# Performance work log

Hardware: AMD Instinct MI355X
Metric: run time of the kernel (lower is better)

## Reference

```python
import jax, jax.numpy as jnp
import numpy as np

NEG_SLOPE = 0.01  # torch.nn.LeakyReLU default


def setup_inputs() -> dict:
    key = jax.random.key(0)
    k1, k2, k3, k4, k5 = jax.random.split(key, 5)
    n_nodes, n_sources, d_in, d_out = 20000, 2048, 128, 128
    x = jax.random.normal(k1, (n_nodes, d_in), dtype=jnp.float32)
    A = jax.random.normal(k2, (n_nodes, n_sources), dtype=jnp.float32)
    W = jax.random.normal(k3, (d_in, d_in), dtype=jnp.float32) * (1.0 / np.sqrt(d_in))
    dense0_w = jax.random.normal(k4, (d_out, d_in), dtype=jnp.float32) * (1.0 / np.sqrt(d_in))
    src_idx = jnp.sort(jax.random.randint(k5, (n_sources,), 0, n_nodes, dtype=jnp.int64))
    return {"x": x, "A": A, "W": W, "dense0_w": dense0_w, "src_idx": src_idx}


def reference(x, A, W, dense0_w, src_idx):
    # GCNConv_Fixed_W: gather source nodes, shared weight transform, adjacency matmul
    support = x[src_idx] @ W                 # [n_sources, d_in]
    out = A @ support                        # [n_nodes, d_in]
    # nonlin + stacked Linear (1 layer, no bias)
    out = jnp.where(out >= 0, out, NEG_SLOPE * out)  # LeakyReLU
    out = out @ dense0_w.T                   # [n_nodes, d_out]
    return out
```

## Files before the change

### kernel.cpp

```cpp
#include <hip/hip_runtime.h>
#include <stdint.h>

#define NNODES 20000
#define NSRC   2048
#define DIN    128
#define BM     80

typedef short s16x8 __attribute__((ext_vector_type(8)));
typedef unsigned short u16x8 __attribute__((ext_vector_type(8)));
typedef float f32x4 __attribute__((ext_vector_type(4)));

static __device__ __forceinline__ unsigned short f2bf(float f) {
  union { float f; unsigned int u; } v; v.f = f;
  unsigned int r = v.u + 0x7FFFu + ((v.u >> 16) & 1u);
  return (unsigned short)(r >> 16);
}

static __device__ __forceinline__ s16x8 pack8(float4 a, float4 b) {
  s16x8 r;
  r[0] = (short)f2bf(a.x); r[1] = (short)f2bf(a.y);
  r[2] = (short)f2bf(a.z); r[3] = (short)f2bf(a.w);
  r[4] = (short)f2bf(b.x); r[5] = (short)f2bf(b.y);
  r[6] = (short)f2bf(b.z); r[7] = (short)f2bf(b.w);
  return r;
}

static __device__ __forceinline__ s16x8 load_cvt8(const float* __restrict__ p) {
  return pack8(*reinterpret_cast<const float4*>(p),
               *reinterpret_cast<const float4*>(p + 4));
}

#define GLL16(g, l)                                                          \
  __builtin_amdgcn_global_load_lds(                                          \
      (const __attribute__((address_space(1))) void*)(g),                    \
      (__attribute__((address_space(3))) void*)(l), 16, 0, 0)

__global__ __launch_bounds__(128) void support_kernel(
    const float* __restrict__ x, const float* __restrict__ W,
    const int* __restrict__ src_idx, unsigned short* __restrict__ supTp) {
  __shared__ float xrows[8][DIN];
  const int j = threadIdx.x;
  const int s0 = blockIdx.x * 8;
#pragma unroll
  for (int i = 0; i < 8; ++i) {
    const int src = src_idx[s0 + i];
    xrows[i][j] = x[(size_t)src * DIN + j];
  }
  __syncthreads();
  float acc[8];
#pragma unroll
  for (int i = 0; i < 8; ++i) acc[i] = 0.f;
  for (int k = 0; k < DIN; ++k) {
    const float w = W[(size_t)k * DIN + j];
#pragma unroll
    for (int i = 0; i < 8; ++i) acc[i] += xrows[i][k] * w;
  }
  u16x8 o;
#pragma unroll
  for (int i = 0; i < 8; ++i) o[i] = f2bf(acc[i]);
  const int kk = s0 >> 5;
  const int g2 = (s0 >> 3) & 3;
  const int n = j >> 4;
  const int lane = (j & 15) + g2 * 16;
  *reinterpret_cast<u16x8*>(&supTp[(size_t)((kk * 8 + n) * 64 + lane) * 8]) = o;
}

__global__ __launch_bounds__(320) void fused_gcn_kernel(
    const float* __restrict__ A,
    const unsigned short* __restrict__ supTp,
    const float* __restrict__ Wd,
    float* __restrict__ out) {
  const int tid = threadIdx.x;
  const int lane = tid & 63;
  const int w = tid >> 6;
  const int r16 = lane & 15;
  const int g = lane >> 4;
  const int rowBase = blockIdx.x * BM;

  __shared__ __attribute__((aligned(16))) unsigned char pool[73728];
  float* Ap = (float*)pool;
  unsigned short* Bp = (unsigned short*)(pool + 40960);

  f32x4 acc[8];
#pragma unroll
  for (int n = 0; n < 8; ++n) acc[n] = (f32x4){0.f, 0.f, 0.f, 0.f};

  const int wu = __builtin_amdgcn_readfirstlane(w);

#define STAGE(buf, c)                                                         \
  {                                                                           \
    _Pragma("unroll") for (int i2 = 0; i2 < 4; ++i2) {                        \
      const int i = w * 4 + i2;                                               \
      const int row = 4 * i + (lane >> 4);                                    \
      GLL16(A + (size_t)(rowBase + row) * NSRC + (c) * 64 +                   \
                (((lane & 15) ^ (row & 7)) << 2),                             \
            Ap + (buf) * 5120 + i * 256);                                     \
    }                                                                         \
    if (wu < 4) {                                                             \
      _Pragma("unroll") for (int i2 = 0; i2 < 4; ++i2) {                      \
        const int iB = w * 4 + i2;                                            \
        GLL16(supTp +                                                         \
                  ((size_t)(((c) * 2 + (iB >> 3)) * 8 + (iB & 7)) * 64 +      \
                   lane) * 8,                                                 \
              Bp + (buf) * 8192 + iB * 512);                                  \
      }                                                                       \
    }                                                                         \
  }

#define COMPUTE(buf)                                                          \
  {                                                                           \
    _Pragma("unroll") for (int kk2 = 0; kk2 < 2; ++kk2) {                     \
      const float* rb = Ap + (buf) * 5120 + (w * 16 + r16) * 64;              \
      const float4 lo = *reinterpret_cast<const float4*>(                     \
          &rb[((kk2 * 8 + g * 2) ^ (r16 & 7)) << 2]);                         \
      const float4 hi = *reinterpret_cast<const float4*>(                     \
          &rb[((kk2 * 8 + g * 2 + 1) ^ (r16 & 7)) << 2]);                     \
      const s16x8 a = pack8(lo, hi);                                          \
      _Pragma("unroll") for (int n = 0; n < 8; ++n) {                         \
        const s16x8 b = *reinterpret_cast<const s16x8*>(                      \
            &Bp[(buf) * 8192 + ((kk2 * 8 + n) * 64 + lane) * 8]);             \
        acc[n] =                                                              \
            __builtin_amdgcn_mfma_f32_16x16x32_bf16(a, b, acc[n], 0, 0, 0);   \
      }                                                                       \
    }                                                                         \
  }

  STAGE(0, 0);
  for (int c = 0; c < 31; ++c) {
    STAGE((c & 1) ^ 1, c + 1);
    if (wu < 4) {
      asm volatile("s_waitcnt vmcnt(8)" ::: "memory");
    } else {
      asm volatile("s_waitcnt vmcnt(4)" ::: "memory");
    }
    __builtin_amdgcn_s_barrier();
    COMPUTE(c & 1);
    __builtin_amdgcn_s_barrier();
  }
  asm volatile("s_waitcnt vmcnt(0)" ::: "memory");
  __builtin_amdgcn_s_barrier();
  COMPUTE(1);

  __builtin_amdgcn_s_barrier();
  unsigned short* actw = (unsigned short*)pool + w * 2176;
#pragma unroll
  for (int n = 0; n < 8; ++n)
#pragma unroll
    for (int r = 0; r < 4; ++r) {
      float v = acc[n][r];
      v = (v >= 0.f) ? v : 0.01f * v;
      actw[(g * 4 + r) * 136 + n * 16 + r16] = f2bf(v);
    }

  f32x4 acc2[8];
#pragma unroll
  for (int n = 0; n < 8; ++n) acc2[n] = (f32x4){0.f, 0.f, 0.f, 0.f};
#pragma unroll
  for (int k2 = 0; k2 < 4; ++k2) {
    const int k = k2 * 32 + g * 8;
    const s16x8 a2 = *reinterpret_cast<const s16x8*>(&actw[r16 * 136 + k]);
#pragma unroll
    for (int n = 0; n < 8; ++n) {
      const s16x8 b2 = load_cvt8(Wd + (size_t)(n * 16 + r16) * DIN + k);
      acc2[n] =
          __builtin_amdgcn_mfma_f32_16x16x32_bf16(a2, b2, acc2[n], 0, 0, 0);
    }
  }
#pragma unroll
  for (int n = 0; n < 8; ++n)
#pragma unroll
    for (int r = 0; r < 4; ++r)
      out[(size_t)(rowBase + w * 16 + g * 4 + r) * DIN + n * 16 + r16] =
          acc2[n][r];
}

extern "C" void kernel_launch(void* const* d_in, const int* in_sizes, int n_in,
                              void* d_out, int out_size, void* d_ws, size_t ws_size,
                              hipStream_t stream) {
  const float* x   = (const float*)d_in[0];
  const float* A   = (const float*)d_in[1];
  const float* W   = (const float*)d_in[2];
  const float* Wd  = (const float*)d_in[3];
  const int*   src = (const int*)d_in[4];
  float* out = (float*)d_out;

  unsigned short* supTp = (unsigned short*)d_ws;

  support_kernel<<<NSRC / 8, 128, 0, stream>>>(x, W, src, supTp);
  fused_gcn_kernel<<<NNODES / BM, 320, 0, stream>>>(A, supTp, Wd, out);
}
```

Measured before the change: 66.55 us.

## Split the A@support K dimension across two blocks and combine in a second kernel

The fused kernel is split into a split-K kernel and a combine kernel. Each of 500 blocks handles half of the 2048-wide K dimension for an 80-row tile, starting at a staggered chunk offset to spread memory traffic. Partial sums are written to workspace as bf16, and a new combine kernel adds the two halves, applies LeakyReLU and runs the dense projection. This doubles the block count from 250 to 500, which helps fill the GPU's compute units. The cost is an extra kernel launch, a workspace round trip, and rounding the partial sums to bf16 before they are added.

```diff
diff --git a/kernel.cpp b/kernel.cpp
--- a/kernel.cpp
+++ b/kernel.cpp
@@ -4,7 +4,8 @@
 #define NNODES 20000
 #define NSRC   2048
 #define DIN    128
-#define BM     80
+#define NTILE  250
+#define TW     5
 
 typedef short s16x8 __attribute__((ext_vector_type(8)));
 typedef unsigned short u16x8 __attribute__((ext_vector_type(8)));
@@ -14,6 +15,11 @@
   union { float f; unsigned int u; } v; v.f = f;
   unsigned int r = v.u + 0x7FFFu + ((v.u >> 16) & 1u);
   return (unsigned short)(r >> 16);
+}
+
+static __device__ __forceinline__ float bf2f(unsigned short u) {
+  union { unsigned int u; float f; } v; v.u = ((unsigned int)u) << 16;
+  return v.f;
 }
 
 static __device__ __forceinline__ s16x8 pack8(float4 a, float4 b) {
@@ -65,17 +71,20 @@
   *reinterpret_cast<u16x8*>(&supTp[(size_t)((kk * 8 + n) * 64 + lane) * 8]) = o;
 }
 
-__global__ __launch_bounds__(320) void fused_gcn_kernel(
+__global__ __launch_bounds__(320) void splitk_kernel(
     const float* __restrict__ A,
     const unsigned short* __restrict__ supTp,
-    const float* __restrict__ Wd,
-    float* __restrict__ out) {
+    unsigned short* __restrict__ pws) {
   const int tid = threadIdx.x;
   const int lane = tid & 63;
   const int w = tid >> 6;
   const int r16 = lane & 15;
   const int g = lane >> 4;
-  const int rowBase = blockIdx.x * BM;
+  const int bid = blockIdx.x;
+  const int tile = bid >> 1;
+  const int half = bid & 1;
+  const int rowBase = tile * 80;
+  const int off = bid & 15;
 
   __shared__ __attribute__((aligned(16))) unsigned char pool[73728];
   float* Ap = (float*)pool;
@@ -87,21 +96,21 @@
 
   const int wu = __builtin_amdgcn_readfirstlane(w);
 
-#define STAGE(buf, c)                                                         \
+#define STAGE(buf, cc)                                                        \
   {                                                                           \
     _Pragma("unroll") for (int i2 = 0; i2 < 4; ++i2) {                        \
-      const int i = w * 4 + i2;                                               \
-      const int row = 4 * i + (lane >> 4);                                    \
-      GLL16(A + (size_t)(rowBase + row) * NSRC + (c) * 64 +                   \
+      const int row = w * 16 + i2 * 4 + (lane >> 4);                          \
+      GLL16(A + (size_t)(rowBase + row) * NSRC + half * 1024 + (cc) * 64 +    \
                 (((lane & 15) ^ (row & 7)) << 2),                             \
-            Ap + (buf) * 5120 + i * 256);                                     \
+            Ap + (buf) * 5120 + w * 1024 + i2 * 256);                         \
     }                                                                         \
     if (wu < 4) {                                                             \
       _Pragma("unroll") for (int i2 = 0; i2 < 4; ++i2) {                      \
         const int iB = w * 4 + i2;                                            \
+        const int C = half * 16 + (cc);                                       \
         GLL16(supTp +                                                         \
-                  ((size_t)(((c) * 2 + (iB >> 3)) * 8 + (iB & 7)) * 64 +      \
-                   lane) * 8,                                                 \
+                  ((size_t)((C * 2 + (iB >> 3)) * 8 + (iB & 7)) * 64 + lane)  \
+                      * 8,                                                    \
               Bp + (buf) * 8192 + iB * 512);                                  \
       }                                                                       \
     }                                                                         \
@@ -125,9 +134,10 @@
     }                                                                         \
   }
 
-  STAGE(0, 0);
-  for (int c = 0; c < 31; ++c) {
-    STAGE((c & 1) ^ 1, c + 1);
+  STAGE(0, off);
+  for (int c = 0; c < 15; ++c) {
+    const int cnext = (c + 1 + off) & 15;
+    STAGE((c & 1) ^ 1, cnext);
     if (wu < 4) {
       asm volatile("s_waitcnt vmcnt(8)" ::: "memory");
     } else {
@@ -141,16 +151,51 @@
   __builtin_amdgcn_s_barrier();
   COMPUTE(1);
 
-  __builtin_amdgcn_s_barrier();
-  unsigned short* actw = (unsigned short*)pool + w * 2176;
-#pragma unroll
-  for (int n = 0; n < 8; ++n)
-#pragma unroll
-    for (int r = 0; r < 4; ++r) {
-      float v = acc[n][r];
-      v = (v >= 0.f) ? v : 0.01f * v;
-      actw[(g * 4 + r) * 136 + n * 16 + r16] = f2bf(v);
-    }
+#pragma unroll
+  for (int n = 0; n < 8; ++n) {
+    ushort4 v;
+    v.x = f2bf(acc[n][0]); v.y = f2bf(acc[n][1]);
+    v.z = f2bf(acc[n][2]); v.w = f2bf(acc[n][3]);
+    const size_t idx =
+        ((((size_t)half * NTILE + tile) * TW + w) * 8 + n) * 64 + lane;
+    *reinterpret_cast<ushort4*>(&pws[idx * 4]) = v;
+  }
+}
+
+__global__ __launch_bounds__(320) void combine_kernel(
+    const unsigned short* __restrict__ pws,
+    const float* __restrict__ Wd,
+    float* __restrict__ out) {
+  const int tid = threadIdx.x;
+  const int lane = tid & 63;
+  const int w = tid >> 6;
+  const int r16 = lane & 15;
+  const int g = lane >> 4;
+  const int tile = blockIdx.x;
+  const int rowBase = tile * 80;
+
+  __shared__ unsigned short act[TW][16 * 136];
+  unsigned short* actw = act[w];
+
+#pragma unroll
+  for (int n = 0; n < 8; ++n) {
+    const size_t i0 = (((size_t)0 * NTILE + tile) * TW + w) * 8 + n;
+    const size_t i1 = (((size_t)1 * NTILE + tile) * TW + w) * 8 + n;
+    const ushort4 h0 = *reinterpret_cast<const ushort4*>(&pws[(i0 * 64 + lane) * 4]);
+    const ushort4 h1 = *reinterpret_cast<const ushort4*>(&pws[(i1 * 64 + lane) * 4]);
+    float v0 = bf2f(h0.x) + bf2f(h1.x);
+    float v1 = bf2f(h0.y) + bf2f(h1.y);
+    float v2 = bf2f(h0.z) + bf2f(h1.z);
+    float v3 = bf2f(h0.w) + bf2f(h1.w);
+    v0 = (v0 >= 0.f) ? v0 : 0.01f * v0;
+    v1 = (v1 >= 0.f) ? v1 : 0.01f * v1;
+    v2 = (v2 >= 0.f) ? v2 : 0.01f * v2;
+    v3 = (v3 >= 0.f) ? v3 : 0.01f * v3;
+    actw[(g * 4 + 0) * 136 + n * 16 + r16] = f2bf(v0);
+    actw[(g * 4 + 1) * 136 + n * 16 + r16] = f2bf(v1);
+    actw[(g * 4 + 2) * 136 + n * 16 + r16] = f2bf(v2);
+    actw[(g * 4 + 3) * 136 + n * 16 + r16] = f2bf(v3);
+  }
 
   f32x4 acc2[8];
 #pragma unroll
@@ -185,7 +230,9 @@
   float* out = (float*)d_out;
 
   unsigned short* supTp = (unsigned short*)d_ws;
+  unsigned short* pws = (unsigned short*)((char*)d_ws + 524288);
 
   support_kernel<<<NSRC / 8, 128, 0, stream>>>(x, W, src, supTp);
-  fused_gcn_kernel<<<NNODES / BM, 320, 0, stream>>>(A, supTp, Wd, out);
-}
+  splitk_kernel<<<NTILE * 2, 320, 0, stream>>>(A, supTp, pws);
+  combine_kernel<<<NTILE, 320, 0, stream>>>(pws, Wd, out);
+}
```

Measured after the change: 71.38 us. 7.3% more time.

## Deepen A/B prefetch to four LDS stages and stagger K-chunk order per block

Applied to the files above, without the earlier changes.

The main GEMM loop moves from double buffering to a four-stage ring of LDS buffers, keeping three chunks of A and support in flight, with vmcnt waits adjusted to match. Each block also walks the 32 K-chunks in an order rotated by its block index, spreading concurrent blocks across different column regions of A and different support tiles. The goal is more latency hiding on the streaming read of A. In exchange, shared memory per block doubles to 144 KiB, which rules out two resident blocks per CU.

```diff
diff --git a/kernel.cpp b/kernel.cpp
--- a/kernel.cpp
+++ b/kernel.cpp
@@ -76,10 +76,11 @@
   const int r16 = lane & 15;
   const int g = lane >> 4;
   const int rowBase = blockIdx.x * BM;
-
-  __shared__ __attribute__((aligned(16))) unsigned char pool[73728];
+  const int off = blockIdx.x & 31;
+
+  __shared__ __attribute__((aligned(16))) unsigned char pool[147456];
   float* Ap = (float*)pool;
-  unsigned short* Bp = (unsigned short*)(pool + 40960);
+  unsigned short* Bp = (unsigned short*)(pool + 81920);
 
   f32x4 acc[8];
 #pragma unroll
@@ -87,20 +88,19 @@
 
   const int wu = __builtin_amdgcn_readfirstlane(w);
 
-#define STAGE(buf, c)                                                         \
+#define STAGE(buf, cc)                                                        \
   {                                                                           \
     _Pragma("unroll") for (int i2 = 0; i2 < 4; ++i2) {                        \
-      const int i = w * 4 + i2;                                               \
-      const int row = 4 * i + (lane >> 4);                                    \
-      GLL16(A + (size_t)(rowBase + row) * NSRC + (c) * 64 +                   \
+      const int row = w * 16 + i2 * 4 + (lane >> 4);                          \
+      GLL16(A + (size_t)(rowBase + row) * NSRC + (cc) * 64 +                  \
                 (((lane & 15) ^ (row & 7)) << 2),                             \
-            Ap + (buf) * 5120 + i * 256);                                     \
+            Ap + (buf) * 5120 + w * 1024 + i2 * 256);                         \
     }                                                                         \
     if (wu < 4) {                                                             \
       _Pragma("unroll") for (int i2 = 0; i2 < 4; ++i2) {                      \
         const int iB = w * 4 + i2;                                            \
         GLL16(supTp +                                                         \
-                  ((size_t)(((c) * 2 + (iB >> 3)) * 8 + (iB & 7)) * 64 +      \
+                  ((size_t)(((cc) * 2 + (iB >> 3)) * 8 + (iB & 7)) * 64 +     \
                    lane) * 8,                                                 \
               Bp + (buf) * 8192 + iB * 512);                                  \
       }                                                                       \
@@ -125,21 +125,35 @@
     }                                                                         \
   }
 
-  STAGE(0, 0);
-  for (int c = 0; c < 31; ++c) {
-    STAGE((c & 1) ^ 1, c + 1);
+#define PERM(i) (((i) + off) & 31)
+
+  STAGE(0, PERM(0));
+  STAGE(1, PERM(1));
+  STAGE(2, PERM(2));
+  for (int c = 0; c < 29; ++c) {
+    STAGE((c + 3) & 3, PERM(c + 3));
     if (wu < 4) {
-      asm volatile("s_waitcnt vmcnt(8)" ::: "memory");
+      asm volatile("s_waitcnt vmcnt(24)" ::: "memory");
     } else {
-      asm volatile("s_waitcnt vmcnt(4)" ::: "memory");
+      asm volatile("s_waitcnt vmcnt(12)" ::: "memory");
     }
     __builtin_amdgcn_s_barrier();
-    COMPUTE(c & 1);
+    COMPUTE(c & 3);
     __builtin_amdgcn_s_barrier();
   }
+  if (wu < 4) { asm volatile("s_waitcnt vmcnt(16)" ::: "memory"); }
+  else        { asm volatile("s_waitcnt vmcnt(8)"  ::: "memory"); }
+  __builtin_amdgcn_s_barrier();
+  COMPUTE(29 & 3);
+  __builtin_amdgcn_s_barrier();
+  if (wu < 4) { asm volatile("s_waitcnt vmcnt(8)" ::: "memory"); }
+  else        { asm volatile("s_waitcnt vmcnt(4)" ::: "memory"); }
+  __builtin_amdgcn_s_barrier();
+  COMPUTE(30 & 3);
+  __builtin_amdgcn_s_barrier();
   asm volatile("s_waitcnt vmcnt(0)" ::: "memory");
   __builtin_amdgcn_s_barrier();
-  COMPUTE(1);
+  COMPUTE(31 & 3);
 
   __builtin_amdgcn_s_barrier();
   unsigned short* actw = (unsigned short*)pool + w * 2176;
```

New measurement: 66.60 us. Within noise of the previous version (+0.1%).
